# Kernel optimization log

Measured on AMD Instinct MI355X. Metric: run time of the kernel, lower is better.

Reference implementation:

```python
import jax, jax.numpy as jnp
import numpy as np
from jax import lax

B, S, T = 64, 64, 32
VE = VD = 32000
E = H = 256
L = 2


def _cell(x, h, c, Wih, Whh, b):
    # PyTorch LSTM gate order: i, f, g, o
    g = x @ Wih.T + h @ Whh.T + b  # [B, 4H]
    i, f, gg, o = jnp.split(g, 4, axis=-1)
    c2 = jax.nn.sigmoid(f) * c + jax.nn.sigmoid(i) * jnp.tanh(gg)
    h2 = jax.nn.sigmoid(o) * jnp.tanh(c2)
    return h2, c2


def _stack_step(x, h, c, Wih, Whh, b):
    # x: [B, E]; h, c: [L, B, H]. Stacked LSTM, dropout is identity at inference.
    hs, cs = [], []
    inp = x
    for l in range(h.shape[0]):
        h2, c2 = _cell(inp, h[l], c[l], Wih[l], Whh[l], b[l])
        hs.append(h2); cs.append(c2)
        inp = h2
    return jnp.stack(hs), jnp.stack(cs), inp


def _encode(tokens, emb, Wih, Whh, b):
    x = emb[tokens]  # [B, S, E]
    bsz = tokens.shape[0]
    h0 = jnp.zeros((L, bsz, H), x.dtype)
    c0 = jnp.zeros((L, bsz, H), x.dtype)

    def step(carry, xt):
        h, c = carry
        h, c, _ = _stack_step(xt, h, c, Wih, Whh, b)
        return (h, c), None

    (h, c), _ = lax.scan(step, (h0, c0), x.transpose(1, 0, 2))
    return h, c


def setup_inputs():
    key = jax.random.key(0)
    ks = jax.random.split(key, 12)
    sd = lambda k, shape: (jax.random.normal(k, shape, dtype=jnp.float32) * 0.05)
    return {
        "input_seq": jax.random.randint(ks[0], (B, S), 0, VE),
        "target_seq": jax.random.randint(ks[1], (B, T), 0, VD),
        "enc_emb": sd(ks[2], (VE, E)),
        "dec_emb": sd(ks[3], (VD, E)),
        "enc_Wih": sd(ks[4], (L, 4 * H, E)),
        "enc_Whh": sd(ks[5], (L, 4 * H, H)),
        "enc_b": sd(ks[6], (L, 4 * H)),
        "dec_Wih": sd(ks[7], (L, 4 * H, E)),
        "dec_Whh": sd(ks[8], (L, 4 * H, H)),
        "dec_b": sd(ks[9], (L, 4 * H)),
        "W_out": sd(ks[10], (VD, H)),
        "b_out": sd(ks[11], (VD,)),
    }


def reference(input_seq, target_seq, enc_emb, dec_emb, enc_Wih, enc_Whh, enc_b,
              dec_Wih, dec_Whh, dec_b, W_out, b_out):
    h, c = _encode(input_seq, enc_emb, enc_Wih, enc_Whh, enc_b)
    bsz, tlen = target_seq.shape
    # dec_in buffer; position 0 is BOS token target_seq[:, 0]; rest filled greedily
    buf0 = jnp.zeros((bsz, tlen), dtype=target_seq.dtype).at[:, 0].set(target_seq[:, 0])
    pos = jnp.arange(tlen)

    def outer(carry, t):
        h, c, buf = carry
        x = dec_emb[buf]  # [B, T, E] -- whole growing prefix re-fed, as in source

        def inner(carry, inp):
            hh, cc = carry
            xt, p = inp
            h2, c2, _ = _stack_step(xt, hh, cc, dec_Wih, dec_Whh, dec_b)
            m = p <= t  # only positions up to current prefix length update state
            hh = jnp.where(m, h2, hh)
            cc = jnp.where(m, c2, cc)
            return (hh, cc), None

        (h, c), _ = lax.scan(inner, (h, c), (x.transpose(1, 0, 2), pos))
        out_top = h[-1]  # LSTM output at last real position t
        pred = out_top @ W_out.T + b_out  # [B, V]
        nxt = jnp.argmax(pred, axis=-1).astype(buf.dtype)
        buf = buf.at[:, t + 1].set(nxt)
        return (h, c, buf), pred

    (_, _, _), preds = lax.scan(outer, (h, c, buf0), jnp.arange(tlen - 1))
    return preds.transpose(1, 0, 2)  # [B, T-1, V]
```

## Files before the change

### kernel.cpp

```cpp
#include <hip/hip_runtime.h>
#include <math.h>


#define B     64
#define SLEN  64
#define TLEN  32
#define HID   256
#define EMBD  256
#define G4    1024
#define VOC   32000
#define NPRED 31
#define FBASE 64

typedef unsigned long long u64;

__device__ __forceinline__ float sigf(float x){ return 1.0f/(1.0f+__expf(-x)); }

__device__ __forceinline__ void gstoref(float* p, float v){
  __hip_atomic_store(p, v, __ATOMIC_RELAXED, __HIP_MEMORY_SCOPE_AGENT);
}
__device__ __forceinline__ void gstorei(int* p, int v){
  __hip_atomic_store(p, v, __ATOMIC_RELAXED, __HIP_MEMORY_SCOPE_AGENT);
}
__device__ __forceinline__ float gloadf(const float* p){
  return __hip_atomic_load(p, __ATOMIC_RELAXED, __HIP_MEMORY_SCOPE_AGENT);
}
__device__ __forceinline__ int gload32(const int* p){
  return __hip_atomic_load(p, __ATOMIC_RELAXED, __HIP_MEMORY_SCOPE_AGENT);
}

__global__ void k_zero(int* __restrict__ p){
  p[threadIdx.x] = 0;
}

__global__ __launch_bounds__(256) void k_tr(const float* __restrict__ src,
                                            float* __restrict__ dst){
  __shared__ float t[64][65];
  const int r0 = blockIdx.x*64, c0 = blockIdx.y*64;
  const int lr = threadIdx.x>>6, lc = threadIdx.x&63;
  #pragma unroll
  for (int i=0;i<16;i++){
    int r = lr + i*4;
    t[r][lc] = src[(size_t)(r0+r)*256 + c0+lc];
  }
  __syncthreads();
  #pragma unroll
  for (int i=0;i<16;i++){
    int c = lr + i*4;
    dst[(size_t)(c0+c)*1024 + r0+lc] = t[lc][c];
  }
}

__global__ __launch_bounds__(256) void k_xproj(
    const int* __restrict__ tok, int tok_stride, int pos0,
    const float* __restrict__ emb, const float* __restrict__ W,
    const float* __restrict__ b0, float* __restrict__ out)
{
  __shared__ float xT[128][64];
  const int tid  = threadIdx.x;
  const int lane = tid & 63;
  const int wv   = __builtin_amdgcn_readfirstlane(tid >> 6);
  const int pos  = pos0 + blockIdx.y;
  const int jbase= blockIdx.x*32 + wv*8;

  const int rS = tid >> 2, klane = tid & 3;
  const int tokrow = tok[rS*tok_stride + pos];
  const float* xsrc = emb + (size_t)tokrow*EMBD;

  float acc[8];
  #pragma unroll
  for (int jj=0;jj<8;jj++) acc[jj]=0.f;

  for (int c=0;c<2;c++){
    __syncthreads();
    #pragma unroll
    for (int i=0;i<32;i++){
      int k = klane + 4*i;
      xT[k][rS] = xsrc[c*128 + k];
    }
    __syncthreads();
    for (int kc=0;kc<8;kc++){
      float x[16];
      #pragma unroll
      for (int i=0;i<16;i++) x[i] = xT[kc*16+i][lane];
      #pragma unroll
      for (int jj=0;jj<8;jj++){
        const float* Wp = W + (size_t)(jbase+jj)*EMBD + c*128 + kc*16;
        float s = 0.f;
        #pragma unroll
        for (int i=0;i<16;i++) s += Wp[i]*x[i];
        acc[jj] += s;
      }
    }
  }
  #pragma unroll
  for (int jj=0;jj<8;jj++){
    int j = jbase+jj;
    out[((size_t)pos*64 + lane)*G4 + j] = acc[jj] + b0[j];
  }
}

__device__ __forceinline__ float4 dotpart(const float4* __restrict__ Wq,
                                          const float* __restrict__ hs,
                                          int kq, int jg){
  float ax=0.f, ay=0.f, az=0.f, aw=0.f;
  const float4* __restrict__ hq = (const float4*)(hs + (kq<<6));
  const float4* __restrict__ w  = Wq + (size_t)(kq<<6)*256 + jg;
  #pragma unroll 4
  for (int kk=0; kk<16; ++kk){
    float4 h4 = hq[kk];
    float4 w0 = w[0];
    float4 w1 = w[256];
    float4 w2 = w[512];
    float4 w3 = w[768];
    ax += w0.x*h4.x; ay += w0.y*h4.x; az += w0.z*h4.x; aw += w0.w*h4.x;
    ax += w1.x*h4.y; ay += w1.y*h4.y; az += w1.z*h4.y; aw += w1.w*h4.y;
    ax += w2.x*h4.z; ay += w2.y*h4.z; az += w2.z*h4.z; aw += w2.w*h4.z;
    ax += w3.x*h4.w; ay += w3.y*h4.w; az += w3.z*h4.w; aw += w3.w*h4.w;
    w += 1024;
  }
  return make_float4(ax,ay,az,aw);
}

__global__ __launch_bounds__(1024) void k_pipe(
    const float* __restrict__ xp, int nsteps,
    const float* __restrict__ WT0, const float* __restrict__ WT1i,
    const float* __restrict__ WT1h, const float* __restrict__ b1,
    float* __restrict__ h0P, float* __restrict__ h1P,
    float* __restrict__ c0P, float* __restrict__ c1P,
    float* __restrict__ h0R, float* __restrict__ p1R,
    int* __restrict__ fA, int* __restrict__ fB1, int* __restrict__ fB2,
    int fbase, int initzero)
{
  __shared__ __align__(16) float part[4][4096];
  __shared__ float xps[1024];
  __shared__ __align__(16) float hloc[256];
  __shared__ float padL[4096];
  const int tid  = threadIdx.x;
  const int kq   = tid >> 8, jg = tid & 255;
  const int role = blockIdx.x >> 6;
  const int r    = blockIdx.x & 63;
  if (nsteps < 0){ padL[tid] = xp[tid]; h0R[tid] = padL[tid ^ 1]; }

  if (role == 0){
    float c0 = 0.f;
    if (tid < HID){
      if (initzero){ c0 = 0.f; hloc[tid] = 0.f; }
      else { c0 = c0P[tid*64 + r]; hloc[tid] = h0P[tid*64 + r]; }
    }
    __syncthreads();
    const float4* W4 = (const float4*)WT0;
    for (int q = 0; q < nsteps; ++q){
      float xv = xp[((size_t)q*64 + r)*G4 + tid];
      if (tid == 0 && q >= 4){
        int tgt = fbase + q - 3, g = 0;
        while (gload32(fB1 + r) < tgt && ++g < (1<<24)) {}
      }
      float4 a = dotpart(W4, hloc, kq, jg);
      xps[tid] = xv;
      *(float4*)&part[kq][jg<<2] = a;
      __syncthreads();
      if (tid < HID){
        float g0 = part[0][tid]+part[1][tid]+part[2][tid]+part[3][tid] + xps[tid];
        float g1 = part[0][HID+tid]+part[1][HID+tid]+part[2][HID+tid]+part[3][HID+tid] + xps[HID+tid];
        float g2 = part[0][2*HID+tid]+part[1][2*HID+tid]+part[2][2*HID+tid]+part[3][2*HID+tid] + xps[2*HID+tid];
        float g3 = part[0][3*HID+tid]+part[1][3*HID+tid]+part[2][3*HID+tid]+part[3][3*HID+tid] + xps[3*HID+tid];
        c0 = sigf(g1)*c0 + sigf(g0)*tanhf(g2);
        float h = sigf(g3)*tanhf(c0);
        hloc[tid] = h;
        gstoref(h0R + (q&3)*16384 + r*256 + tid, h);
        asm volatile("s_waitcnt vmcnt(0)" ::: "memory");
      }
      __syncthreads();
      if (tid == 0) gstorei(fA + r, fbase + q + 1);
    }
    if (tid < HID){ c0P[tid*64 + r] = c0; h0P[tid*64 + r] = hloc[tid]; }
  }
  else if (role == 1){
    const float4* W4 = (const float4*)WT1i;
    for (int q = 0; q < nsteps; ++q){
      if (tid == 0){
        int tgt = fbase + q + 1, g = 0;
        while (gload32(fA + r) < tgt && ++g < (1<<24)) {}
        if (q >= 4){
          int t2 = fbase + q - 3; g = 0;
          while (gload32(fB2 + r) < t2 && ++g < (1<<24)) {}
        }
      }
      __syncthreads();
      if (tid < HID) hloc[tid] = gloadf(h0R + (q&3)*16384 + r*256 + tid);
      __syncthreads();
      float4 a = dotpart(W4, hloc, kq, jg);
      *(float4*)&part[kq][jg<<2] = a;
      __syncthreads();
      float p = part[0][tid]+part[1][tid]+part[2][tid]+part[3][tid];
      gstoref(p1R + (q&3)*65536 + r*1024 + tid, p);
      asm volatile("s_waitcnt vmcnt(0)" ::: "memory");
      __syncthreads();
      if (tid == 0) gstorei(fB1 + r, fbase + q + 1);
    }
  }
  else {
    float c1 = 0.f, bb0=0.f, bb1=0.f, bb2=0.f, bb3=0.f;
    if (tid < HID){
      bb0 = b1[tid]; bb1 = b1[HID+tid]; bb2 = b1[2*HID+tid]; bb3 = b1[3*HID+tid];
      if (initzero){ c1 = 0.f; hloc[tid] = 0.f; }
      else { c1 = c1P[tid*64 + r]; hloc[tid] = h1P[tid*64 + r]; }
    }
    __syncthreads();
    const float4* W4 = (const float4*)WT1h;
    for (int q = 0; q < nsteps; ++q){
      if (tid == 0){
        int tgt = fbase + q + 1, g = 0;
        while (gload32(fB1 + r) < tgt && ++g < (1<<24)) {}
      }
      __syncthreads();
      xps[tid] = gloadf(p1R + (q&3)*65536 + r*1024 + tid);
      asm volatile("s_waitcnt vmcnt(0)" ::: "memory");
      __syncthreads();
      if (tid == 0) gstorei(fB2 + r, fbase + q + 1);
      float4 a = dotpart(W4, hloc, kq, jg);
      *(float4*)&part[kq][jg<<2] = a;
      __syncthreads();
      if (tid < HID){
        float g0 = part[0][tid]+part[1][tid]+part[2][tid]+part[3][tid] + xps[tid] + bb0;
        float g1 = part[0][HID+tid]+part[1][HID+tid]+part[2][HID+tid]+part[3][HID+tid] + xps[HID+tid] + bb1;
        float g2 = part[0][2*HID+tid]+part[1][2*HID+tid]+part[2][2*HID+tid]+part[3][2*HID+tid] + xps[2*HID+tid] + bb2;
        float g3 = part[0][3*HID+tid]+part[1][3*HID+tid]+part[2][3*HID+tid]+part[3][3*HID+tid] + xps[3*HID+tid] + bb3;
        c1 = sigf(g1)*c1 + sigf(g0)*tanhf(g2);
        float h = sigf(g3)*tanhf(c1);
        hloc[tid] = h;
        if (q == nsteps-1) h1P[tid*64 + r] = h;
      }
      __syncthreads();
    }
    if (tid < HID) c1P[tid*64 + r] = c1;
  }
}

__global__ __launch_bounds__(1024) void k_megadec(
    float* xp,
    const float* __restrict__ WT0, const float* __restrict__ WT1i,
    const float* __restrict__ WT1h, const float* __restrict__ b1,
    const float* __restrict__ Wih0, const float* __restrict__ b0,
    const float* __restrict__ emb,
    const float* __restrict__ Wout, const float* __restrict__ bout,
    float* __restrict__ dout,
    const float* __restrict__ h0P, const float* __restrict__ h1P,
    const float* __restrict__ c0P, const float* __restrict__ c1P,
    float* __restrict__ h0R, float* __restrict__ p1R, float* __restrict__ h1R,
    float* __restrict__ pPv, int* __restrict__ pPi, float* __restrict__ xeG,
    int* __restrict__ flags)
{
  __shared__ __align__(16) float part[4][4096];
  __shared__ float xps[1024];
  __shared__ __align__(16) float hloc[256];
  __shared__ int   iscr[1024];
  __shared__ float htp[256*65];

  int* fA = flags;        int* fB1 = flags + 64;  int* fB2 = flags + 128;
  int* fH = flags + 192;  int* fP  = flags + 256; int* fX  = flags + 320;
  int* fT = flags + 384;

  const int tid  = threadIdx.x;
  const int lane = tid & 63;
  const int wv   = __builtin_amdgcn_readfirstlane(tid >> 6);
  const int kq   = tid >> 8, jg = tid & 255;
  const int xcd  = blockIdx.x & 7;
  const int role = xcd >> 1;
  const int r    = ((xcd & 1) << 5) | (blockIdx.x >> 3);

  if (role == 0){
    float c0 = 0.f;
    if (tid < HID){ c0 = c0P[tid*64 + r]; hloc[tid] = h0P[tid*64 + r]; }
    __syncthreads();
    const float4* W4 = (const float4*)WT0;
    int cum = 0;
    for (int t = 0; t < NPRED; ++t)
    for (int p = 0; p <= t; ++p, ++cum){
      if (wv == 0){
        if (lane == 0 && cum >= 4){
          int tgt = FBASE + cum - 3, g = 0;
          while (gload32(fB1 + r) < tgt && ++g < (1<<24)) {}
        }
        if (p == t && t >= 1){
          int g = 0;
          while (!__all(gload32(fX + lane) >= t) && ++g < (1<<24)) {}
        }
      }
      __syncthreads();
      const float* xa = xp + ((size_t)p*64 + r)*G4 + tid;
      float xv = (p == t) ? gloadf(xa) : *xa;
      float4 a = dotpart(W4, hloc, kq, jg);
      xps[tid] = xv;
      *(float4*)&part[kq][jg<<2] = a;
      __syncthreads();
      if (tid < HID){
        float g0 = part[0][tid]+part[1][tid]+part[2][tid]+part[3][tid] + xps[tid];
        float g1 = part[0][HID+tid]+part[1][HID+tid]+part[2][HID+tid]+part[3][HID+tid] + xps[HID+tid];
        float g2 = part[0][2*HID+tid]+part[1][2*HID+tid]+part[2][2*HID+tid]+part[3][2*HID+tid] + xps[2*HID+tid];
        float g3 = part[0][3*HID+tid]+part[1][3*HID+tid]+part[2][3*HID+tid]+part[3][3*HID+tid] + xps[3*HID+tid];
        c0 = sigf(g1)*c0 + sigf(g0)*tanhf(g2);
        float h = sigf(g3)*tanhf(c0);
        hloc[tid] = h;
        gstoref(h0R + (cum&3)*16384 + r*256 + tid, h);
        asm volatile("s_waitcnt vmcnt(0)" ::: "memory");
      }
      __syncthreads();
      if (tid == 0) gstorei(fA + r, FBASE + cum + 1);
    }
  }
  else if (role == 1){
    const float4* W4 = (const float4*)WT1i;
    int cum = 0;
    for (int t = 0; t < NPRED; ++t)
    for (int p = 0; p <= t; ++p, ++cum){
      if (tid == 0){
        int tgt = FBASE + cum + 1, g = 0;
        while (gload32(fA + r) < tgt && ++g < (1<<24)) {}
        if (cum >= 4){
          int t2 = FBASE + cum - 3; g = 0;
          while (gload32(fB2 + r) < t2 && ++g < (1<<24)) {}
        }
      }
      __syncthreads();
      if (tid < HID) hloc[tid] = gloadf(h0R + (cum&3)*16384 + r*256 + tid);
      __syncthreads();
      float4 a = dotpart(W4, hloc, kq, jg);
      *(float4*)&part[kq][jg<<2] = a;
      __syncthreads();
      float pp = part[0][tid]+part[1][tid]+part[2][tid]+part[3][tid];
      gstoref(p1R + (cum&3)*65536 + r*1024 + tid, pp);
      asm volatile("s_waitcnt vmcnt(0)" ::: "memory");
      __syncthreads();
      if (tid == 0) gstorei(fB1 + r, FBASE + cum + 1);
    }
  }
  else if (role == 2){
    float c1 = 0.f, bb0=0.f, bb1=0.f, bb2=0.f, bb3=0.f;
    if (tid < HID){
      bb0 = b1[tid]; bb1 = b1[HID+tid]; bb2 = b1[2*HID+tid]; bb3 = b1[3*HID+tid];
      c1 = c1P[tid*64 + r]; hloc[tid] = h1P[tid*64 + r];
    }
    __syncthreads();
    const float4* W4 = (const float4*)WT1h;
    int cum = 0;
    for (int t = 0; t < NPRED; ++t)
    for (int p = 0; p <= t; ++p, ++cum){
      if (tid == 0){
        int tgt = FBASE + cum + 1, g = 0;
        while (gload32(fB1 + r) < tgt && ++g < (1<<24)) {}
      }
      __syncthreads();
      xps[tid] = gloadf(p1R + (cum&3)*65536 + r*1024 + tid);
      asm volatile("s_waitcnt vmcnt(0)" ::: "memory");
      __syncthreads();
      if (tid == 0) gstorei(fB2 + r, FBASE + cum + 1);
      float4 a = dotpart(W4, hloc, kq, jg);
      *(float4*)&part[kq][jg<<2] = a;
      __syncthreads();
      if (tid < HID){
        float g0 = part[0][tid]+part[1][tid]+part[2][tid]+part[3][tid] + xps[tid] + bb0;
        float g1 = part[0][HID+tid]+part[1][HID+tid]+part[2][HID+tid]+part[3][HID+tid] + xps[HID+tid] + bb1;
        float g2 = part[0][2*HID+tid]+part[1][2*HID+tid]+part[2][2*HID+tid]+part[3][2*HID+tid] + xps[2*HID+tid] + bb2;
        float g3 = part[0][3*HID+tid]+part[1][3*HID+tid]+part[2][3*HID+tid]+part[3][3*HID+tid] + xps[3*HID+tid] + bb3;
        c1 = sigf(g1)*c1 + sigf(g0)*tanhf(g2);
        float h = sigf(g3)*tanhf(c1);
        hloc[tid] = h;
      }
      __syncthreads();
      if (p == t){
        if (tid == 0 && t >= 2){
          int g = 0;
          while (gload32(fT) < t - 1 && ++g < (1<<24)) {}
        }
        __syncthreads();
        if (tid < HID){
          gstoref(h1R + (t&1)*16384 + r*256 + tid, hloc[tid]);
          asm volatile("s_waitcnt vmcnt(0)" ::: "memory");
        }
        __syncthreads();
        if (tid == 0) gstorei(fH + r, t + 1);
      }
    }
  }
  else {
    const int v  = r;
    const int v0 = v * 500;
    const int rr = tid >> 4;
    const int jl = tid & 15;
    const float b0v = b0[v*16 + jl];

    for (int t = 0; t < NPRED; ++t){
      if (wv == 0){
        int g = 0;
        while (!__all(gload32(fH + lane) >= t+1) && ++g < (1<<24))
          __builtin_amdgcn_s_sleep(4);
      }
      if (tid == 0 && t >= 2){
        int g = 0;
        while (gload32(fT) < t - 1 && ++g < (1<<24)) {}
      }
      __syncthreads();
      {
        const float* src = h1R + (size_t)(t&1)*16384;
        #pragma unroll
        for (int i=0;i<16;i++){
          int idx = tid + i*1024;
          float vl = gloadf(src + idx);
          htp[(idx & 255)*65 + (idx >> 8)] = vl;
        }
      }
      __syncthreads();
      float best = -INFINITY; int bi = 0x7fffffff;
      for (int ib = 0; ib < 4; ++ib){
        float acc[8];
        #pragma unroll
        for (int jj=0;jj<8;jj++){
          int i = ib*8+jj;
          acc[jj] = (wv + 16*i < 500) ? bout[v0 + wv + 16*i] : 0.f;
        }
        for (int kc = 0; kc < 16; ++kc){
          float x[16];
          #pragma unroll
          for (int u=0;u<16;u++) x[u] = htp[(kc*16+u)*65 + lane];
          #pragma unroll
          for (int jj=0;jj<8;jj++){
            int i = ib*8+jj;
            if (wv + 16*i < 500){
              const float* Wp = Wout + (size_t)(v0 + wv + 16*i)*HID + kc*16;
              #pragma unroll
              for (int u=0;u<16;u++) acc[jj] += Wp[u]*x[u];
            }
          }
        }
        #pragma unroll
        for (int jj=0;jj<8;jj++){
          int i = ib*8+jj;
          if (wv + 16*i < 500){
            int vv = v0 + wv + 16*i;
            dout[((size_t)lane*NPRED + t)*VOC + vv] = acc[jj];
            if (acc[jj] > best){ best = acc[jj]; bi = vv; }
          }
        }
      }
      xps[wv*64 + lane] = best; iscr[wv*64 + lane] = bi;
      __syncthreads();
      if (wv == 0){
        float bb = xps[lane]; int bbi = iscr[lane];
        #pragma unroll
        for (int w=1; w<16; w++){
          float vl = xps[w*64+lane]; int ii = iscr[w*64+lane];
          if (vl > bb || (vl == bb && ii < bbi)){ bb = vl; bbi = ii; }
        }
        gstoref(pPv + (t&1)*4096 + v*64 + lane, bb);
        gstorei(pPi + (t&1)*4096 + v*64 + lane, bbi);
        asm volatile("s_waitcnt vmcnt(0)" ::: "memory");
      }
      __syncthreads();
      if (tid == 0) gstorei(fP + v, t + 1);
      if (t == NPRED-1) continue;

      if (v == 0){
        if (wv == 0){
          int g = 0;
          while (!__all(gload32(fP + lane) >= t+1) && ++g < (1<<24)) {}
        }
        __syncthreads();
        {
          float bb = -INFINITY; int bbi = 0x7fffffff;
          #pragma unroll
          for (int i=0;i<4;i++){
            int vs = wv*4 + i;
            float vl = gloadf(pPv + (t&1)*4096 + vs*64 + lane);
            int  ii  = gload32(pPi + (t&1)*4096 + vs*64 + lane);
            if (vl > bb || (vl == bb && ii < bbi)){ bb = vl; bbi = ii; }
          }
          xps[wv*64+lane] = bb; iscr[wv*64+lane] = bbi;
        }
        __syncthreads();
        if (wv == 0){
          float bb = xps[lane]; int bbi = iscr[lane];
          #pragma unroll
          for (int w=1; w<16; w++){
            float vl = xps[w*64+lane]; int ii = iscr[w*64+lane];
            if (vl > bb || (vl == bb && ii < bbi)){ bb = vl; bbi = ii; }
          }
          iscr[lane] = bbi;
        }
        __syncthreads();
        {
          int tk = iscr[tid & 63];
          int r2 = tid & 63, kb = (tid >> 6) * 16;
          const float* er = emb + (size_t)tk*EMBD + kb;
          #pragma unroll
          for (int i=0;i<16;i++) gstoref(xeG + (kb+i)*64 + r2, er[i]);
          asm volatile("s_waitcnt vmcnt(0)" ::: "memory");
        }
        __syncthreads();
        if (tid == 0) gstorei(fT, t + 1);
      }

      if (tid == 0){
        int g = 0;
        while (gload32(fT) < t + 1 && ++g < (1<<24))
          __builtin_amdgcn_s_sleep(2);
      }
      __syncthreads();
      {
        #pragma unroll
        for (int i=0;i<16;i++){
          int idx = tid + i*1024;
          htp[(idx >> 6)*65 + (idx & 63)] = gloadf(xeG + idx);
        }
      }
      __syncthreads();
      {
        int j  = v*16 + jl;
        const float* Wj = Wih0 + (size_t)j*EMBD;
        float acc = b0v;
        #pragma unroll 16
        for (int k=0;k<256;k++) acc += Wj[k]*htp[k*65 + rr];
        gstoref(xp + ((size_t)(t+1)*64 + rr)*G4 + v*16 + jl, acc);
        asm volatile("s_waitcnt vmcnt(0)" ::: "memory");
      }
      __syncthreads();
      if (tid == 0) gstorei(fX + v, t + 1);
    }
  }
}

extern "C" void kernel_launch(void* const* d_in, const int* in_sizes, int n_in,
                              void* d_out, int out_size, void* d_ws, size_t ws_size,
                              hipStream_t stream)
{
  const int*   input_seq  = (const int*)d_in[0];
  const int*   target_seq = (const int*)d_in[1];
  const float* enc_emb = (const float*)d_in[2];
  const float* dec_emb = (const float*)d_in[3];
  const float* enc_Wih = (const float*)d_in[4];
  const float* enc_Whh = (const float*)d_in[5];
  const float* enc_b   = (const float*)d_in[6];
  const float* dec_Wih = (const float*)d_in[7];
  const float* dec_Whh = (const float*)d_in[8];
  const float* dec_b   = (const float*)d_in[9];
  const float* W_out   = (const float*)d_in[10];
  const float* b_out   = (const float*)d_in[11];
  float* out = (float*)d_out;

  float* ws   = (float*)d_ws;
  float* xp_e = ws;
  float* xp_d = xp_e + (size_t)SLEN*64*G4;
  float* h0P  = xp_d + (size_t)TLEN*64*G4;
  float* h1P  = h0P + HID*64;
  float* c0P  = h1P + HID*64;
  float* c1P  = c0P + HID*64;
  float* h0R  = c1P + HID*64;
  float* p1R  = h0R + 4*16384;
  float* h1R  = p1R + 4*65536;
  float* pPv  = h1R + 2*16384;
  int*   pPi  = (int*)(pPv + 2*4096);
  float* xeG  = (float*)(pPi + 2*4096);
  int*   flags= (int*)(xeG + 16384);
  float* WT0  = (float*)(flags + 512);
  float* WT1i = WT0  + HID*G4;
  float* WT1h = WT1i + HID*G4;

  k_zero<<<1, 512, 0, stream>>>(flags);

  dim3 trg(16, 4);
  k_tr<<<trg, 256, 0, stream>>>(enc_Whh,                   WT0);
  k_tr<<<trg, 256, 0, stream>>>(enc_Wih + (size_t)G4*EMBD, WT1i);
  k_tr<<<trg, 256, 0, stream>>>(enc_Whh + (size_t)G4*HID,  WT1h);
  k_xproj<<<dim3(32, SLEN), 256, 0, stream>>>(input_seq, SLEN, 0, enc_emb,
        enc_Wih, enc_b, xp_e);
  k_pipe<<<192, 1024, 0, stream>>>(xp_e, SLEN,
        WT0, WT1i, WT1h, enc_b + G4,
        h0P, h1P, c0P, c1P, h0R, p1R,
        flags, flags + 64, flags + 128, 0, 1);

  k_tr<<<trg, 256, 0, stream>>>(dec_Whh,                   WT0);
  k_tr<<<trg, 256, 0, stream>>>(dec_Wih + (size_t)G4*EMBD, WT1i);
  k_tr<<<trg, 256, 0, stream>>>(dec_Whh + (size_t)G4*HID,  WT1h);
  k_xproj<<<dim3(32, 1), 256, 0, stream>>>(target_seq, TLEN, 0, dec_emb,
        dec_Wih, dec_b, xp_d);

  k_megadec<<<256, 1024, 0, stream>>>(xp_d,
        WT0, WT1i, WT1h, dec_b + G4,
        dec_Wih, dec_b, dec_emb, W_out, b_out, out,
        h0P, h1P, c0P, c1P,
        h0R, p1R, h1R, pPv, pPi, xeG, flags);
}
```

Baseline: 8.881 ms.

## Process two batch rows per recurrent block and decentralize argmax/embedding gather

The decoder megakernel's three recurrent roles now each handle two batch rows per block. A new dual dot-product loads the weight tile once and applies it to both hidden vectors, which halves the blocks per role (16 instead of 32 per XCD pair) and halves redundant weight streaming. The central token-selection step is removed: every projection block waits on all partial argmax flags, reduces the 64 partials itself, and gathers the embedding directly. This drops the fT flag and the xeG round trip, but every block now repeats the reduction. Shared memory is unioned between the recurrent and projection roles to fit the larger partial buffers.

```diff
diff --git a/kernel.cpp b/kernel.cpp
--- a/kernel.cpp
+++ b/kernel.cpp
@@ -120,6 +120,34 @@
     w += 1024;
   }
   return make_float4(ax,ay,az,aw);
+}
+
+__device__ __forceinline__ void dotpart2(const float4* __restrict__ Wq,
+    const float* __restrict__ ha, const float* __restrict__ hb,
+    int kq, int jg, float4& A, float4& Bv){
+  float ax=0.f,ay=0.f,az=0.f,aw=0.f, bx=0.f,by=0.f,bz=0.f,bw=0.f;
+  const float4* __restrict__ hqa = (const float4*)(ha + (kq<<6));
+  const float4* __restrict__ hqb = (const float4*)(hb + (kq<<6));
+  const float4* __restrict__ w   = Wq + (size_t)(kq<<6)*256 + jg;
+  #pragma unroll 2
+  for (int kk=0; kk<16; ++kk){
+    float4 h4a = hqa[kk], h4b = hqb[kk];
+    float4 w0 = w[0];
+    float4 w1 = w[256];
+    float4 w2 = w[512];
+    float4 w3 = w[768];
+    ax += w0.x*h4a.x; ay += w0.y*h4a.x; az += w0.z*h4a.x; aw += w0.w*h4a.x;
+    ax += w1.x*h4a.y; ay += w1.y*h4a.y; az += w1.z*h4a.y; aw += w1.w*h4a.y;
+    ax += w2.x*h4a.z; ay += w2.y*h4a.z; az += w2.z*h4a.z; aw += w2.w*h4a.z;
+    ax += w3.x*h4a.w; ay += w3.y*h4a.w; az += w3.z*h4a.w; aw += w3.w*h4a.w;
+    bx += w0.x*h4b.x; by += w0.y*h4b.x; bz += w0.z*h4b.x; bw += w0.w*h4b.x;
+    bx += w1.x*h4b.y; by += w1.y*h4b.y; bz += w1.z*h4b.y; bw += w1.w*h4b.y;
+    bx += w2.x*h4b.z; by += w2.y*h4b.z; bz += w2.z*h4b.z; bw += w2.w*h4b.z;
+    bx += w3.x*h4b.w; by += w3.y*h4b.w; bz += w3.z*h4b.w; bw += w3.w*h4b.w;
+    w += 1024;
+  }
+  A  = make_float4(ax,ay,az,aw);
+  Bv = make_float4(bx,by,bz,bw);
 }
 
 __global__ __launch_bounds__(1024) void k_pipe(
@@ -249,30 +277,42 @@
     const float* __restrict__ h0P, const float* __restrict__ h1P,
     const float* __restrict__ c0P, const float* __restrict__ c1P,
     float* __restrict__ h0R, float* __restrict__ p1R, float* __restrict__ h1R,
-    float* __restrict__ pPv, int* __restrict__ pPi, float* __restrict__ xeG,
+    float* __restrict__ pPv, int* __restrict__ pPi,
     int* __restrict__ flags)
 {
-  __shared__ __align__(16) float part[4][4096];
-  __shared__ float xps[1024];
-  __shared__ __align__(16) float hloc[256];
-  __shared__ int   iscr[1024];
-  __shared__ float htp[256*65];
+  __shared__ union {
+    struct {
+      float part[8][4096];
+      float xps[2][1024];
+      float hloc[2][256];
+    } c;
+    struct {
+      float htp[256*65];
+      float red[1024];
+      int   idx[1024];
+      int   tok[64];
+    } p;
+  } S;
 
   int* fA = flags;        int* fB1 = flags + 64;  int* fB2 = flags + 128;
   int* fH = flags + 192;  int* fP  = flags + 256; int* fX  = flags + 320;
-  int* fT = flags + 384;
 
   const int tid  = threadIdx.x;
   const int lane = tid & 63;
   const int wv   = __builtin_amdgcn_readfirstlane(tid >> 6);
   const int kq   = tid >> 8, jg = tid & 255;
   const int xcd  = blockIdx.x & 7;
-  const int role = xcd >> 1;
-  const int r    = ((xcd & 1) << 5) | (blockIdx.x >> 3);
+  const int slot = blockIdx.x >> 3;
+  if (xcd < 6 && slot >= 16) return;
+  const int role = (xcd < 6) ? (xcd >> 1) : 3;
+  const int w    = ((xcd & 1) << 4) | slot;
+  const int v    = ((xcd & 1) << 5) | slot;
 
   if (role == 0){
+    const int r0 = 2*w, r1 = 2*w+1;
+    const int u = tid >> 1, row = tid & 1, rr = 2*w + row;
     float c0 = 0.f;
-    if (tid < HID){ c0 = c0P[tid*64 + r]; hloc[tid] = h0P[tid*64 + r]; }
+    if (tid < 512){ c0 = c0P[u*64 + rr]; S.c.hloc[row][u] = h0P[u*64 + rr]; }
     __syncthreads();
     const float4* W4 = (const float4*)WT0;
     int cum = 0;
@@ -281,7 +321,7 @@
       if (wv == 0){
         if (lane == 0 && cum >= 4){
           int tgt = FBASE + cum - 3, g = 0;
-          while (gload32(fB1 + r) < tgt && ++g < (1<<24)) {}
+          while (gload32(fB1 + w) < tgt && ++g < (1<<24)) {}
         }
         if (p == t && t >= 1){
           int g = 0;
@@ -289,58 +329,68 @@
         }
       }
       __syncthreads();
-      const float* xa = xp + ((size_t)p*64 + r)*G4 + tid;
-      float xv = (p == t) ? gloadf(xa) : *xa;
-      float4 a = dotpart(W4, hloc, kq, jg);
-      xps[tid] = xv;
-      *(float4*)&part[kq][jg<<2] = a;
-      __syncthreads();
-      if (tid < HID){
-        float g0 = part[0][tid]+part[1][tid]+part[2][tid]+part[3][tid] + xps[tid];
-        float g1 = part[0][HID+tid]+part[1][HID+tid]+part[2][HID+tid]+part[3][HID+tid] + xps[HID+tid];
-        float g2 = part[0][2*HID+tid]+part[1][2*HID+tid]+part[2][2*HID+tid]+part[3][2*HID+tid] + xps[2*HID+tid];
-        float g3 = part[0][3*HID+tid]+part[1][3*HID+tid]+part[2][3*HID+tid]+part[3][3*HID+tid] + xps[3*HID+tid];
+      const float* xa0 = xp + ((size_t)p*64 + r0)*G4 + tid;
+      const float* xa1 = xp + ((size_t)p*64 + r1)*G4 + tid;
+      float xv0 = (p == t) ? gloadf(xa0) : *xa0;
+      float xv1 = (p == t) ? gloadf(xa1) : *xa1;
+      float4 a, bv;
+      dotpart2(W4, S.c.hloc[0], S.c.hloc[1], kq, jg, a, bv);
+      S.c.xps[0][tid] = xv0; S.c.xps[1][tid] = xv1;
+      *(float4*)&S.c.part[kq*2+0][jg<<2] = a;
+      *(float4*)&S.c.part[kq*2+1][jg<<2] = bv;
+      __syncthreads();
+      if (tid < 512){
+        float g0 = S.c.part[row][u]      +S.c.part[2+row][u]      +S.c.part[4+row][u]      +S.c.part[6+row][u]      + S.c.xps[row][u];
+        float g1 = S.c.part[row][HID+u]  +S.c.part[2+row][HID+u]  +S.c.part[4+row][HID+u]  +S.c.part[6+row][HID+u]  + S.c.xps[row][HID+u];
+        float g2 = S.c.part[row][2*HID+u]+S.c.part[2+row][2*HID+u]+S.c.part[4+row][2*HID+u]+S.c.part[6+row][2*HID+u]+ S.c.xps[row][2*HID+u];
+        float g3 = S.c.part[row][3*HID+u]+S.c.part[2+row][3*HID+u]+S.c.part[4+row][3*HID+u]+S.c.part[6+row][3*HID+u]+ S.c.xps[row][3*HID+u];
         c0 = sigf(g1)*c0 + sigf(g0)*tanhf(g2);
         float h = sigf(g3)*tanhf(c0);
-        hloc[tid] = h;
-        gstoref(h0R + (cum&3)*16384 + r*256 + tid, h);
+        S.c.hloc[row][u] = h;
+        gstoref(h0R + (cum&3)*16384 + rr*256 + u, h);
         asm volatile("s_waitcnt vmcnt(0)" ::: "memory");
       }
       __syncthreads();
-      if (tid == 0) gstorei(fA + r, FBASE + cum + 1);
+      if (tid == 0) gstorei(fA + w, FBASE + cum + 1);
     }
   }
   else if (role == 1){
+    const int u = tid >> 1, row = tid & 1, rr = 2*w + row;
     const float4* W4 = (const float4*)WT1i;
     int cum = 0;
     for (int t = 0; t < NPRED; ++t)
     for (int p = 0; p <= t; ++p, ++cum){
       if (tid == 0){
         int tgt = FBASE + cum + 1, g = 0;
-        while (gload32(fA + r) < tgt && ++g < (1<<24)) {}
+        while (gload32(fA + w) < tgt && ++g < (1<<24)) {}
         if (cum >= 4){
           int t2 = FBASE + cum - 3; g = 0;
-          while (gload32(fB2 + r) < t2 && ++g < (1<<24)) {}
-        }
-      }
-      __syncthreads();
-      if (tid < HID) hloc[tid] = gloadf(h0R + (cum&3)*16384 + r*256 + tid);
-      __syncthreads();
-      float4 a = dotpart(W4, hloc, kq, jg);
-      *(float4*)&part[kq][jg<<2] = a;
-      __syncthreads();
-      float pp = part[0][tid]+part[1][tid]+part[2][tid]+part[3][tid];
-      gstoref(p1R + (cum&3)*65536 + r*1024 + tid, pp);
+          while (gload32(fB2 + w) < t2 && ++g < (1<<24)) {}
+        }
+      }
+      __syncthreads();
+      if (tid < 512) S.c.hloc[row][u] = gloadf(h0R + (cum&3)*16384 + rr*256 + u);
+      __syncthreads();
+      float4 a, bv;
+      dotpart2(W4, S.c.hloc[0], S.c.hloc[1], kq, jg, a, bv);
+      *(float4*)&S.c.part[kq*2+0][jg<<2] = a;
+      *(float4*)&S.c.part[kq*2+1][jg<<2] = bv;
+      __syncthreads();
+      float pp0 = S.c.part[0][tid]+S.c.part[2][tid]+S.c.part[4][tid]+S.c.part[6][tid];
+      float pp1 = S.c.part[1][tid]+S.c.part[3][tid]+S.c.part[5][tid]+S.c.part[7][tid];
+      gstoref(p1R + (cum&3)*65536 + (size_t)(2*w)*1024   + tid, pp0);
+      gstoref(p1R + (cum&3)*65536 + (size_t)(2*w+1)*1024 + tid, pp1);
       asm volatile("s_waitcnt vmcnt(0)" ::: "memory");
       __syncthreads();
-      if (tid == 0) gstorei(fB1 + r, FBASE + cum + 1);
+      if (tid == 0) gstorei(fB1 + w, FBASE + cum + 1);
     }
   }
   else if (role == 2){
+    const int u = tid >> 1, row = tid & 1, rr = 2*w + row;
     float c1 = 0.f, bb0=0.f, bb1=0.f, bb2=0.f, bb3=0.f;
-    if (tid < HID){
-      bb0 = b1[tid]; bb1 = b1[HID+tid]; bb2 = b1[2*HID+tid]; bb3 = b1[3*HID+tid];
-      c1 = c1P[tid*64 + r]; hloc[tid] = h1P[tid*64 + r];
+    if (tid < 512){
+      bb0 = b1[u]; bb1 = b1[HID+u]; bb2 = b1[2*HID+u]; bb3 = b1[3*HID+u];
+      c1 = c1P[u*64 + rr]; S.c.hloc[row][u] = h1P[u*64 + rr];
     }
     __syncthreads();
     const float4* W4 = (const float4*)WT1h;
@@ -349,43 +399,48 @@
     for (int p = 0; p <= t; ++p, ++cum){
       if (tid == 0){
         int tgt = FBASE + cum + 1, g = 0;
-        while (gload32(fB1 + r) < tgt && ++g < (1<<24)) {}
-      }
-      __syncthreads();
-      xps[tid] = gloadf(p1R + (cum&3)*65536 + r*1024 + tid);
+        while (gload32(fB1 + w) < tgt && ++g < (1<<24)) {}
+      }
+      __syncthreads();
+      S.c.xps[0][tid] = gloadf(p1R + (cum&3)*65536 + (size_t)(2*w)*1024   + tid);
+      S.c.xps[1][tid] = gloadf(p1R + (cum&3)*65536 + (size_t)(2*w+1)*1024 + tid);
       asm volatile("s_waitcnt vmcnt(0)" ::: "memory");
       __syncthreads();
-      if (tid == 0) gstorei(fB2 + r, FBASE + cum + 1);
-      float4 a = dotpart(W4, hloc, kq, jg);
-      *(float4*)&part[kq][jg<<2] = a;
-      __syncthreads();
-      if (tid < HID){
-        float g0 = part[0][tid]+part[1][tid]+part[2][tid]+part[3][tid] + xps[tid] + bb0;
-        float g1 = part[0][HID+tid]+part[1][HID+tid]+part[2][HID+tid]+part[3][HID+tid] + xps[HID+tid] + bb1;
-        float g2 = part[0][2*HID+tid]+part[1][2*HID+tid]+part[2][2*HID+tid]+part[3][2*HID+tid] + xps[2*HID+tid] + bb2;
-        float g3 = part[0][3*HID+tid]+part[1][3*HID+tid]+part[2][3*HID+tid]+part[3][3*HID+tid] + xps[3*HID+tid] + bb3;
+      if (tid == 0) gstorei(fB2 + w, FBASE + cum + 1);
+      float4 a, bv;
+      dotpart2(W4, S.c.hloc[0], S.c.hloc[1], kq, jg, a, bv);
+      *(float4*)&S.c.part[kq*2+0][jg<<2] = a;
+      *(float4*)&S.c.part[kq*2+1][jg<<2] = bv;
+      __syncthreads();
+      if (tid < 512){
+        float g0 = S.c.part[row][u]      +S.c.part[2+row][u]      +S.c.part[4+row][u]      +S.c.part[6+row][u]      + S.c.xps[row][u]       + bb0;
+        float g1 = S.c.part[row][HID+u]  +S.c.part[2+row][HID+u]  +S.c.part[4+row][HID+u]  +S.c.part[6+row][HID+u]  + S.c.xps[row][HID+u]   + bb1;
+        float g2 = S.c.part[row][2*HID+u]+S.c.part[2+row][2*HID+u]+S.c.part[4+row][2*HID+u]+S.c.part[6+row][2*HID+u]+ S.c.xps[row][2*HID+u] + bb2;
+        float g3 = S.c.part[row][3*HID+u]+S.c.part[2+row][3*HID+u]+S.c.part[4+row][3*HID+u]+S.c.part[6+row][3*HID+u]+ S.c.xps[row][3*HID+u] + bb3;
         c1 = sigf(g1)*c1 + sigf(g0)*tanhf(g2);
         float h = sigf(g3)*tanhf(c1);
-        hloc[tid] = h;
+        S.c.hloc[row][u] = h;
       }
       __syncthreads();
       if (p == t){
-        if (tid == 0 && t >= 2){
+        if (wv == 0 && t >= 2){
           int g = 0;
-          while (gload32(fT) < t - 1 && ++g < (1<<24)) {}
+          while (!__all(gload32(fP + lane) >= t-1) && ++g < (1<<24)) {}
         }
         __syncthreads();
-        if (tid < HID){
-          gstoref(h1R + (t&1)*16384 + r*256 + tid, hloc[tid]);
+        if (tid < 512){
+          gstoref(h1R + (t&1)*16384 + rr*256 + u, S.c.hloc[row][u]);
           asm volatile("s_waitcnt vmcnt(0)" ::: "memory");
         }
         __syncthreads();
-        if (tid == 0) gstorei(fH + r, t + 1);
+        if (tid == 0){
+          gstorei(fH + 2*w,   t + 1);
+          gstorei(fH + 2*w+1, t + 1);
+        }
       }
     }
   }
   else {
-    const int v  = r;
     const int v0 = v * 500;
     const int rr = tid >> 4;
     const int jl = tid & 15;
@@ -396,10 +451,6 @@
         int g = 0;
         while (!__all(gload32(fH + lane) >= t+1) && ++g < (1<<24))
           __builtin_amdgcn_s_sleep(4);
-      }
-      if (tid == 0 && t >= 2){
-        int g = 0;
-        while (gload32(fT) < t - 1 && ++g < (1<<24)) {}
       }
       __syncthreads();
       {
@@ -408,7 +459,7 @@
         for (int i=0;i<16;i++){
           int idx = tid + i*1024;
           float vl = gloadf(src + idx);
-          htp[(idx & 255)*65 + (idx >> 8)] = vl;
+          S.p.htp[(idx & 255)*65 + (idx >> 8)] = vl;
         }
       }
       __syncthreads();
@@ -423,14 +474,14 @@
         for (int kc = 0; kc < 16; ++kc){
           float x[16];
           #pragma unroll
-          for (int u=0;u<16;u++) x[u] = htp[(kc*16+u)*65 + lane];
+          for (int u2=0;u2<16;u2++) x[u2] = S.p.htp[(kc*16+u2)*65 + lane];
           #pragma unroll
           for (int jj=0;jj<8;jj++){
             int i = ib*8+jj;
             if (wv + 16*i < 500){
               const float* Wp = Wout + (size_t)(v0 + wv + 16*i)*HID + kc*16;
               #pragma unroll
-              for (int u=0;u<16;u++) acc[jj] += Wp[u]*x[u];
+              for (int u2=0;u2<16;u2++) acc[jj] += Wp[u2]*x[u2];
             }
           }
         }
@@ -444,13 +495,13 @@
           }
         }
       }
-      xps[wv*64 + lane] = best; iscr[wv*64 + lane] = bi;
+      S.p.red[wv*64 + lane] = best; S.p.idx[wv*64 + lane] = bi;
       __syncthreads();
       if (wv == 0){
-        float bb = xps[lane]; int bbi = iscr[lane];
+        float bb = S.p.red[lane]; int bbi = S.p.idx[lane];
         #pragma unroll
-        for (int w=1; w<16; w++){
-          float vl = xps[w*64+lane]; int ii = iscr[w*64+lane];
+        for (int w2=1; w2<16; w2++){
+          float vl = S.p.red[w2*64+lane]; int ii = S.p.idx[w2*64+lane];
           if (vl > bb || (vl == bb && ii < bbi)){ bb = vl; bbi = ii; }
         }
         gstoref(pPv + (t&1)*4096 + v*64 + lane, bb);
@@ -461,66 +512,34 @@
       if (tid == 0) gstorei(fP + v, t + 1);
       if (t == NPRED-1) continue;
 
-      if (v == 0){
-        if (wv == 0){
-          int g = 0;
-          while (!__all(gload32(fP + lane) >= t+1) && ++g < (1<<24)) {}
-        }
-        __syncthreads();
-        {
-          float bb = -INFINITY; int bbi = 0x7fffffff;
-          #pragma unroll
-          for (int i=0;i<4;i++){
-            int vs = wv*4 + i;
-            float vl = gloadf(pPv + (t&1)*4096 + vs*64 + lane);
-            int  ii  = gload32(pPi + (t&1)*4096 + vs*64 + lane);
-            if (vl > bb || (vl == bb && ii < bbi)){ bb = vl; bbi = ii; }
-          }
-          xps[wv*64+lane] = bb; iscr[wv*64+lane] = bbi;
-        }
-        __syncthreads();
-        if (wv == 0){
-          float bb = xps[lane]; int bbi = iscr[lane];
-          #pragma unroll
-          for (int w=1; w<16; w++){
-            float vl = xps[w*64+lane]; int ii = iscr[w*64+lane];
-            if (vl > bb || (vl == bb && ii < bbi)){ bb = vl; bbi = ii; }
-          }
-          iscr[lane] = bbi;
-        }
-        __syncthreads();
-        {
-          int tk = iscr[tid & 63];
-          int r2 = tid & 63, kb = (tid >> 6) * 16;
-          const float* er = emb + (size_t)tk*EMBD + kb;
-          #pragma unroll
-          for (int i=0;i<16;i++) gstoref(xeG + (kb+i)*64 + r2, er[i]);
-          asm volatile("s_waitcnt vmcnt(0)" ::: "memory");
-        }
-        __syncthreads();
-        if (tid == 0) gstorei(fT, t + 1);
-      }
-
-      if (tid == 0){
+      if (wv == 0){
         int g = 0;
-        while (gload32(fT) < t + 1 && ++g < (1<<24))
-          __builtin_amdgcn_s_sleep(2);
+        while (!__all(gload32(fP + lane) >= t+1) && ++g < (1<<24)) {}
+        float bb = -INFINITY; int bbi = 0x7fffffff;
+        for (int vs = 0; vs < 64; ++vs){
+          float vl = gloadf(pPv + (t&1)*4096 + vs*64 + lane);
+          int  ii  = gload32(pPi + (t&1)*4096 + vs*64 + lane);
+          if (vl > bb || (vl == bb && ii < bbi)){ bb = vl; bbi = ii; }
+        }
+        S.p.tok[lane] = bbi;
       }
       __syncthreads();
       {
         #pragma unroll
         for (int i=0;i<16;i++){
           int idx = tid + i*1024;
-          htp[(idx >> 6)*65 + (idx & 63)] = gloadf(xeG + idx);
+          int k2 = idx >> 6, r2 = idx & 63;
+          int tk = S.p.tok[r2];
+          S.p.htp[k2*65 + r2] = emb[(size_t)tk*EMBD + k2];
         }
       }
       __syncthreads();
       {
-        int j  = v*16 + jl;
+        int j = v*16 + jl;
         const float* Wj = Wih0 + (size_t)j*EMBD;
         float acc = b0v;
         #pragma unroll 16
-        for (int k=0;k<256;k++) acc += Wj[k]*htp[k*65 + rr];
+        for (int k2=0;k2<256;k2++) acc += Wj[k2]*S.p.htp[k2*65 + rr];
         gstoref(xp + ((size_t)(t+1)*64 + rr)*G4 + v*16 + jl, acc);
         asm volatile("s_waitcnt vmcnt(0)" ::: "memory");
       }
@@ -560,8 +579,7 @@
   float* h1R  = p1R + 4*65536;
   float* pPv  = h1R + 2*16384;
   int*   pPi  = (int*)(pPv + 2*4096);
-  float* xeG  = (float*)(pPi + 2*4096);
-  int*   flags= (int*)(xeG + 16384);
+  int*   flags= (int*)(pPi + 2*4096);
   float* WT0  = (float*)(flags + 512);
   float* WT1i = WT0  + HID*G4;
   float* WT1h = WT1i + HID*G4;
@@ -589,5 +607,5 @@
         WT0, WT1i, WT1h, dec_b + G4,
         dec_Wih, dec_b, dec_emb, W_out, b_out, out,
         h0P, h1P, c0P, c1P,
-        h0R, p1R, h1R, pPv, pPi, xeG, flags);
-}
+        h0R, p1R, h1R, pPv, pPi, flags);
+}
```

Measured after the change: 9.399 ms. 5.8% more time.

## Pad sync flags per cache line and decentralize argmax/embedding gather

Applied to the files above, without the earlier changes.

Flag arrays are spread out with a stride of 16 ints so each block's flag sits on its own 64-byte line, which is meant to cut false sharing during spin-polling. The single block that reduced the argmax partials, gathered the embeddings into a global buffer and raised one global flag is gone. Every x-projection block now does the 64-way argmax reduction itself and gathers its embedding rows directly, which removes one serialized handoff and a global round trip from each decode step. The price is redundant reduction and gather work in every block. The role-2 blocks now wait on the per-block prediction flags instead.

```diff
diff --git a/kernel.cpp b/kernel.cpp
--- a/kernel.cpp
+++ b/kernel.cpp
@@ -11,6 +11,7 @@
 #define VOC   32000
 #define NPRED 31
 #define FBASE 64
+#define FS    16
 
 typedef unsigned long long u64;
 
@@ -30,7 +31,7 @@
 }
 
 __global__ void k_zero(int* __restrict__ p){
-  p[threadIdx.x] = 0;
+  p[blockIdx.x*1024 + threadIdx.x] = 0;
 }
 
 __global__ __launch_bounds__(256) void k_tr(const float* __restrict__ src,
@@ -154,7 +155,7 @@
       float xv = xp[((size_t)q*64 + r)*G4 + tid];
       if (tid == 0 && q >= 4){
         int tgt = fbase + q - 3, g = 0;
-        while (gload32(fB1 + r) < tgt && ++g < (1<<24)) {}
+        while (gload32(fB1 + r*FS) < tgt && ++g < (1<<24)) {}
       }
       float4 a = dotpart(W4, hloc, kq, jg);
       xps[tid] = xv;
@@ -172,7 +173,7 @@
         asm volatile("s_waitcnt vmcnt(0)" ::: "memory");
       }
       __syncthreads();
-      if (tid == 0) gstorei(fA + r, fbase + q + 1);
+      if (tid == 0) gstorei(fA + r*FS, fbase + q + 1);
     }
     if (tid < HID){ c0P[tid*64 + r] = c0; h0P[tid*64 + r] = hloc[tid]; }
   }
@@ -181,10 +182,10 @@
     for (int q = 0; q < nsteps; ++q){
       if (tid == 0){
         int tgt = fbase + q + 1, g = 0;
-        while (gload32(fA + r) < tgt && ++g < (1<<24)) {}
+        while (gload32(fA + r*FS) < tgt && ++g < (1<<24)) {}
         if (q >= 4){
           int t2 = fbase + q - 3; g = 0;
-          while (gload32(fB2 + r) < t2 && ++g < (1<<24)) {}
+          while (gload32(fB2 + r*FS) < t2 && ++g < (1<<24)) {}
         }
       }
       __syncthreads();
@@ -197,7 +198,7 @@
       gstoref(p1R + (q&3)*65536 + r*1024 + tid, p);
       asm volatile("s_waitcnt vmcnt(0)" ::: "memory");
       __syncthreads();
-      if (tid == 0) gstorei(fB1 + r, fbase + q + 1);
+      if (tid == 0) gstorei(fB1 + r*FS, fbase + q + 1);
     }
   }
   else {
@@ -212,13 +213,13 @@
     for (int q = 0; q < nsteps; ++q){
       if (tid == 0){
         int tgt = fbase + q + 1, g = 0;
-        while (gload32(fB1 + r) < tgt && ++g < (1<<24)) {}
+        while (gload32(fB1 + r*FS) < tgt && ++g < (1<<24)) {}
       }
       __syncthreads();
       xps[tid] = gloadf(p1R + (q&3)*65536 + r*1024 + tid);
       asm volatile("s_waitcnt vmcnt(0)" ::: "memory");
       __syncthreads();
-      if (tid == 0) gstorei(fB2 + r, fbase + q + 1);
+      if (tid == 0) gstorei(fB2 + r*FS, fbase + q + 1);
       float4 a = dotpart(W4, hloc, kq, jg);
       *(float4*)&part[kq][jg<<2] = a;
       __syncthreads();
@@ -249,7 +250,7 @@
     const float* __restrict__ h0P, const float* __restrict__ h1P,
     const float* __restrict__ c0P, const float* __restrict__ c1P,
     float* __restrict__ h0R, float* __restrict__ p1R, float* __restrict__ h1R,
-    float* __restrict__ pPv, int* __restrict__ pPi, float* __restrict__ xeG,
+    float* __restrict__ pPv, int* __restrict__ pPi,
     int* __restrict__ flags)
 {
   __shared__ __align__(16) float part[4][4096];
@@ -258,9 +259,8 @@
   __shared__ int   iscr[1024];
   __shared__ float htp[256*65];
 
-  int* fA = flags;        int* fB1 = flags + 64;  int* fB2 = flags + 128;
-  int* fH = flags + 192;  int* fP  = flags + 256; int* fX  = flags + 320;
-  int* fT = flags + 384;
+  int* fA = flags;          int* fB1 = flags + 1024;  int* fB2 = flags + 2048;
+  int* fH = flags + 3072;   int* fP  = flags + 4096;  int* fX  = flags + 5120;
 
   const int tid  = threadIdx.x;
   const int lane = tid & 63;
@@ -281,11 +281,11 @@
       if (wv == 0){
         if (lane == 0 && cum >= 4){
           int tgt = FBASE + cum - 3, g = 0;
-          while (gload32(fB1 + r) < tgt && ++g < (1<<24)) {}
+          while (gload32(fB1 + r*FS) < tgt && ++g < (1<<24)) {}
         }
         if (p == t && t >= 1){
           int g = 0;
-          while (!__all(gload32(fX + lane) >= t) && ++g < (1<<24)) {}
+          while (!__all(gload32(fX + lane*FS) >= t) && ++g < (1<<24)) {}
         }
       }
       __syncthreads();
@@ -307,7 +307,7 @@
         asm volatile("s_waitcnt vmcnt(0)" ::: "memory");
       }
       __syncthreads();
-      if (tid == 0) gstorei(fA + r, FBASE + cum + 1);
+      if (tid == 0) gstorei(fA + r*FS, FBASE + cum + 1);
     }
   }
   else if (role == 1){
@@ -317,10 +317,10 @@
     for (int p = 0; p <= t; ++p, ++cum){
       if (tid == 0){
         int tgt = FBASE + cum + 1, g = 0;
-        while (gload32(fA + r) < tgt && ++g < (1<<24)) {}
+        while (gload32(fA + r*FS) < tgt && ++g < (1<<24)) {}
         if (cum >= 4){
           int t2 = FBASE + cum - 3; g = 0;
-          while (gload32(fB2 + r) < t2 && ++g < (1<<24)) {}
+          while (gload32(fB2 + r*FS) < t2 && ++g < (1<<24)) {}
         }
       }
       __syncthreads();
@@ -333,7 +333,7 @@
       gstoref(p1R + (cum&3)*65536 + r*1024 + tid, pp);
       asm volatile("s_waitcnt vmcnt(0)" ::: "memory");
       __syncthreads();
-      if (tid == 0) gstorei(fB1 + r, FBASE + cum + 1);
+      if (tid == 0) gstorei(fB1 + r*FS, FBASE + cum + 1);
     }
   }
   else if (role == 2){
@@ -349,13 +349,13 @@
     for (int p = 0; p <= t; ++p, ++cum){
       if (tid == 0){
         int tgt = FBASE + cum + 1, g = 0;
-        while (gload32(fB1 + r) < tgt && ++g < (1<<24)) {}
+        while (gload32(fB1 + r*FS) < tgt && ++g < (1<<24)) {}
       }
       __syncthreads();
       xps[tid] = gloadf(p1R + (cum&3)*65536 + r*1024 + tid);
       asm volatile("s_waitcnt vmcnt(0)" ::: "memory");
       __syncthreads();
-      if (tid == 0) gstorei(fB2 + r, FBASE + cum + 1);
+      if (tid == 0) gstorei(fB2 + r*FS, FBASE + cum + 1);
       float4 a = dotpart(W4, hloc, kq, jg);
       *(float4*)&part[kq][jg<<2] = a;
       __syncthreads();
@@ -372,7 +372,11 @@
       if (p == t){
         if (tid == 0 && t >= 2){
           int g = 0;
-          while (gload32(fT) < t - 1 && ++g < (1<<24)) {}
+          while (gload32(fP) < t - 1 && ++g < (1<<24)) {}
+        }
+        if (wv == 1 && t >= 2){
+          int g = 0;
+          while (!__all(gload32(fP + lane*FS) >= t-1) && ++g < (1<<24)) {}
         }
         __syncthreads();
         if (tid < HID){
@@ -380,7 +384,7 @@
           asm volatile("s_waitcnt vmcnt(0)" ::: "memory");
         }
         __syncthreads();
-        if (tid == 0) gstorei(fH + r, t + 1);
+        if (tid == 0) gstorei(fH + r*FS, t + 1);
       }
     }
   }
@@ -394,12 +398,8 @@
     for (int t = 0; t < NPRED; ++t){
       if (wv == 0){
         int g = 0;
-        while (!__all(gload32(fH + lane) >= t+1) && ++g < (1<<24))
-          __builtin_amdgcn_s_sleep(4);
-      }
-      if (tid == 0 && t >= 2){
-        int g = 0;
-        while (gload32(fT) < t - 1 && ++g < (1<<24)) {}
+        while (!__all(gload32(fH + lane*FS) >= t+1) && ++g < (1<<24))
+          __builtin_amdgcn_s_sleep(8);
       }
       __syncthreads();
       {
@@ -458,74 +458,42 @@
         asm volatile("s_waitcnt vmcnt(0)" ::: "memory");
       }
       __syncthreads();
-      if (tid == 0) gstorei(fP + v, t + 1);
+      if (tid == 0) gstorei(fP + v*FS, t + 1);
       if (t == NPRED-1) continue;
 
-      if (v == 0){
-        if (wv == 0){
-          int g = 0;
-          while (!__all(gload32(fP + lane) >= t+1) && ++g < (1<<24)) {}
-        }
-        __syncthreads();
-        {
-          float bb = -INFINITY; int bbi = 0x7fffffff;
-          #pragma unroll
-          for (int i=0;i<4;i++){
-            int vs = wv*4 + i;
-            float vl = gloadf(pPv + (t&1)*4096 + vs*64 + lane);
-            int  ii  = gload32(pPi + (t&1)*4096 + vs*64 + lane);
-            if (vl > bb || (vl == bb && ii < bbi)){ bb = vl; bbi = ii; }
-          }
-          xps[wv*64+lane] = bb; iscr[wv*64+lane] = bbi;
-        }
-        __syncthreads();
-        if (wv == 0){
-          float bb = xps[lane]; int bbi = iscr[lane];
-          #pragma unroll
-          for (int w=1; w<16; w++){
-            float vl = xps[w*64+lane]; int ii = iscr[w*64+lane];
-            if (vl > bb || (vl == bb && ii < bbi)){ bb = vl; bbi = ii; }
-          }
-          iscr[lane] = bbi;
-        }
-        __syncthreads();
-        {
-          int tk = iscr[tid & 63];
-          int r2 = tid & 63, kb = (tid >> 6) * 16;
-          const float* er = emb + (size_t)tk*EMBD + kb;
-          #pragma unroll
-          for (int i=0;i<16;i++) gstoref(xeG + (kb+i)*64 + r2, er[i]);
-          asm volatile("s_waitcnt vmcnt(0)" ::: "memory");
-        }
-        __syncthreads();
-        if (tid == 0) gstorei(fT, t + 1);
-      }
-
-      if (tid == 0){
+      if (wv == 0){
         int g = 0;
-        while (gload32(fT) < t + 1 && ++g < (1<<24))
-          __builtin_amdgcn_s_sleep(2);
+        while (!__all(gload32(fP + lane*FS) >= t+1) && ++g < (1<<24)) {}
+        float bb = -INFINITY; int bbi = 0x7fffffff;
+        for (int vs = 0; vs < 64; ++vs){
+          float vl = gloadf(pPv + (t&1)*4096 + vs*64 + lane);
+          int  ii  = gload32(pPi + (t&1)*4096 + vs*64 + lane);
+          if (vl > bb || (vl == bb && ii < bbi)){ bb = vl; bbi = ii; }
+        }
+        iscr[lane] = bbi;
       }
       __syncthreads();
       {
         #pragma unroll
         for (int i=0;i<16;i++){
           int idx = tid + i*1024;
-          htp[(idx >> 6)*65 + (idx & 63)] = gloadf(xeG + idx);
+          int k2 = idx >> 6, r2 = idx & 63;
+          int tk = iscr[r2];
+          htp[k2*65 + r2] = emb[(size_t)tk*EMBD + k2];
         }
       }
       __syncthreads();
       {
-        int j  = v*16 + jl;
+        int j = v*16 + jl;
         const float* Wj = Wih0 + (size_t)j*EMBD;
         float acc = b0v;
         #pragma unroll 16
-        for (int k=0;k<256;k++) acc += Wj[k]*htp[k*65 + rr];
+        for (int k2=0;k2<256;k2++) acc += Wj[k2]*htp[k2*65 + rr];
         gstoref(xp + ((size_t)(t+1)*64 + rr)*G4 + v*16 + jl, acc);
         asm volatile("s_waitcnt vmcnt(0)" ::: "memory");
       }
       __syncthreads();
-      if (tid == 0) gstorei(fX + v, t + 1);
+      if (tid == 0) gstorei(fX + v*FS, t + 1);
     }
   }
 }
@@ -560,13 +528,12 @@
   float* h1R  = p1R + 4*65536;
   float* pPv  = h1R + 2*16384;
   int*   pPi  = (int*)(pPv + 2*4096);
-  float* xeG  = (float*)(pPi + 2*4096);
-  int*   flags= (int*)(xeG + 16384);
-  float* WT0  = (float*)(flags + 512);
+  int*   flags= (int*)(pPi + 2*4096);
+  float* WT0  = (float*)(flags + 6144);
   float* WT1i = WT0  + HID*G4;
   float* WT1h = WT1i + HID*G4;
 
-  k_zero<<<1, 512, 0, stream>>>(flags);
+  k_zero<<<6, 1024, 0, stream>>>(flags);
 
   dim3 trg(16, 4);
   k_tr<<<trg, 256, 0, stream>>>(enc_Whh,                   WT0);
@@ -577,7 +544,7 @@
   k_pipe<<<192, 1024, 0, stream>>>(xp_e, SLEN,
         WT0, WT1i, WT1h, enc_b + G4,
         h0P, h1P, c0P, c1P, h0R, p1R,
-        flags, flags + 64, flags + 128, 0, 1);
+        flags, flags + 1024, flags + 2048, 0, 1);
 
   k_tr<<<trg, 256, 0, stream>>>(dec_Whh,                   WT0);
   k_tr<<<trg, 256, 0, stream>>>(dec_Wih + (size_t)G4*EMBD, WT1i);
@@ -589,5 +556,5 @@
         WT0, WT1i, WT1h, dec_b + G4,
         dec_Wih, dec_b, dec_emb, W_out, b_out, out,
         h0P, h1P, c0P, c1P,
-        h0R, p1R, h1R, pPv, pPi, xeG, flags);
-}
+        h0R, p1R, h1R, pPv, pPi, flags);
+}
```

Measured after the change: 9.060 ms. +2.0%, slower.
